# Kernel optimization log

Hardware: AMD Instinct MI355X
Metric: run time of the kernel (lower is better)

The kernel has to match this reference:

```python
import jax, jax.numpy as jnp
import numpy as np

B, C, W, H = 4, 256, 64, 64
D = C // 8  # reduced query/key channels


def setup_inputs() -> dict:
    key = jax.random.key(0)
    k1, k2, k3, k4, k5 = jax.random.split(key, 5)
    return {
        "x": jax.random.normal(k1, (B, C, W, H), dtype=jnp.float32),
        "q_weight": jax.random.normal(k2, (D, C), dtype=jnp.float32) * 0.05,
        "k_weight": jax.random.normal(k3, (D, C), dtype=jnp.float32) * 0.05,
        "v_weight": jax.random.normal(k4, (C, C), dtype=jnp.float32) * 0.05,
        "gamma": jax.random.normal(k5, (1,), dtype=jnp.float32),
    }


def reference(x, q_weight, k_weight, v_weight, gamma):
    b, c, w, h = x.shape
    n = w * h
    xf = x.reshape(b, c, n)                       # (B, C, N)
    # 1x1 convs == channel matmuls
    q = jnp.einsum('dc,bcn->bdn', q_weight, xf)   # (B, D, N)
    k = jnp.einsum('dc,bcn->bdn', k_weight, xf)   # (B, D, N)
    v = jnp.einsum('oc,bcn->bon', v_weight, xf)   # (B, C, N)
    # energy[b, i, j] = <q[:, i], k[:, j]>  (unscaled, single head)
    energy = jnp.einsum('bdi,bdj->bij', q, k)     # (B, N, N)
    attn = jax.nn.softmax(energy, axis=-1)        # softmax over keys j
    # out[b, c, i] = sum_j v[b, c, j] * attn[b, i, j]
    out = jnp.einsum('bcj,bij->bci', v, attn)     # (B, C, N)
    out = out.reshape(b, c, w, h)
    return gamma[0] * out + x
```

## Files before the change

kernel.cpp:

```cpp
#include <hip/hip_runtime.h>
#include <math.h>

#define Bb 4
#define Cc 256
#define Nn 4096
#define Dd 32
#define CH 128
#define XST 264

typedef __attribute__((ext_vector_type(8))) short bf16x8;
typedef __attribute__((ext_vector_type(4))) float f32x4;

__device__ __forceinline__ unsigned short f2bf(float x) {
    union { float f; unsigned u; } c; c.f = x;
    unsigned r = c.u + 0x7fffu + ((c.u >> 16) & 1u);
    return (unsigned short)(r >> 16);
}
__device__ __forceinline__ unsigned pk2(float a, float b) {
    return (unsigned)f2bf(a) | ((unsigned)f2bf(b) << 16);
}
__device__ __forceinline__ void load_lds16(const void* g, void* l) {
    __builtin_amdgcn_global_load_lds(
        (const __attribute__((address_space(1))) void*)g,
        (__attribute__((address_space(3))) void*)l, 16, 0, 0);
}
__device__ __forceinline__ float fexp2(float x) {
#if __has_builtin(__builtin_amdgcn_exp2f)
    return __builtin_amdgcn_exp2f(x);
#else
    return __exp2f(x);
#endif
}
template <int CTRL>
__device__ __forceinline__ float dppf(float v) {
    int iv = __builtin_bit_cast(int, v);
    return __builtin_bit_cast(float,
        __builtin_amdgcn_update_dpp(iv, iv, CTRL, 0xF, 0xF, false));
}
__device__ __forceinline__ float rowsum16(float v) {
    v += dppf<0xB1>(v);
    v += dppf<0x4E>(v);
    v += dppf<0x141>(v);
    v += dppf<0x140>(v);
    return v;
}

__global__ __launch_bounds__(256) void pack_w(
    const float* __restrict__ qw, const float* __restrict__ kw,
    const float* __restrict__ vw, short* __restrict__ wpk) {
    const int g = blockIdx.x * 256 + threadIdx.x;
    const int qd = g & 3, m = (g >> 2) & 15, kc = (g >> 6) & 7, ot = g >> 9;
    const int o = 16 * ot + m;
    const float* src;
    float scale = 1.0f;
    if (o < 32)      { src = qw + (size_t)o * Cc; scale = 1.44269504088896f; }
    else if (o < 64) { src = kw + (size_t)(o - 32) * Cc; }
    else             { src = vw + (size_t)(o - 64) * Cc; }
    const float* s8 = src + 32 * kc + 8 * qd;
    uint4 u;
    u.x = pk2(s8[0] * scale, s8[1] * scale);
    u.y = pk2(s8[2] * scale, s8[3] * scale);
    u.z = pk2(s8[4] * scale, s8[5] * scale);
    u.w = pk2(s8[6] * scale, s8[7] * scale);
    *(uint4*)(wpk + (size_t)g * 8) = u;
}

__global__ __launch_bounds__(256) void proj(
    const float* __restrict__ x, const short* __restrict__ wpk,
    short* __restrict__ q_t, short* __restrict__ k_t, short* __restrict__ v_b) {
    __shared__ alignas(16) short xs[32 * XST];
    const int b = blockIdx.z;
    const int n0 = blockIdx.x * 32;
    const int tid = threadIdx.x;
    const int w = tid >> 6;
    const int lane = tid & 63, qd = lane >> 4, m = lane & 15;

    {
        const int n = tid & 31, cg = tid >> 5;
        const float* xp = x + ((size_t)b * Cc + 32 * cg) * Nn + n0 + n;
        float xv[32];
#pragma unroll
        for (int i = 0; i < 32; ++i) xv[i] = xp[(size_t)i * Nn];
        short* row = xs + n * XST + 32 * cg;
#pragma unroll
        for (int u4 = 0; u4 < 4; ++u4)
            *(uint4*)(row + 8 * u4) = make_uint4(
                pk2(xv[8*u4+0], xv[8*u4+1]), pk2(xv[8*u4+2], xv[8*u4+3]),
                pk2(xv[8*u4+4], xv[8*u4+5]), pk2(xv[8*u4+6], xv[8*u4+7]));
    }
    __syncthreads();

    const int fslot = m * 4 + qd;
    f32x4 acc[5][2];
#pragma unroll
    for (int i = 0; i < 5; ++i)
#pragma unroll
        for (int nt = 0; nt < 2; ++nt) acc[i][nt] = (f32x4){0.f, 0.f, 0.f, 0.f};

    bf16x8 afc[5], afn[5];
#pragma unroll
    for (int i = 0; i < 5; ++i)
        afc[i] = *(const bf16x8*)(wpk + ((size_t)((4*i + w) * 8 + 0) * 64 + fslot) * 8);

    for (int kc = 0; kc < 8; ++kc) {
        if (kc < 7) {
#pragma unroll
            for (int i = 0; i < 5; ++i)
                afn[i] = *(const bf16x8*)(
                    wpk + ((size_t)((4*i + w) * 8 + kc + 1) * 64 + fslot) * 8);
        }
        const bf16x8 b0 = *(const bf16x8*)&xs[(     m) * XST + 32 * kc + 8 * qd];
        const bf16x8 b1 = *(const bf16x8*)&xs[(16 + m) * XST + 32 * kc + 8 * qd];
#pragma unroll
        for (int i = 0; i < 5; ++i)
            acc[i][0] = __builtin_amdgcn_mfma_f32_16x16x32_bf16(afc[i], b0, acc[i][0], 0, 0, 0);
#pragma unroll
        for (int i = 0; i < 5; ++i)
            acc[i][1] = __builtin_amdgcn_mfma_f32_16x16x32_bf16(afc[i], b1, acc[i][1], 0, 0, 0);
#pragma unroll
        for (int i = 0; i < 5; ++i) afc[i] = afn[i];
    }

#pragma unroll
    for (int i = 0; i < 5; ++i) {
        const int ot = 4 * i + w;
        if (ot < 4) {
            short* dst = (ot < 2 ? q_t : k_t) + (size_t)b * Nn * Dd;
            const int dbase = (ot & 1) * 16 + 4 * qd;
#pragma unroll
            for (int nt = 0; nt < 2; ++nt) {
                const f32x4 a = acc[i][nt];
                *(uint2*)(dst + (size_t)(n0 + 16 * nt + m) * Dd + dbase) =
                    make_uint2(pk2(a[0], a[1]), pk2(a[2], a[3]));
            }
        } else {
            const int cbase = (ot - 4) * 16 + 4 * qd;
            const int gbase = n0 & ~63;
            const int off2 = (n0 & 32) ? 2 : 0;
#pragma unroll
            for (int rr = 0; rr < 4; ++rr) {
                const unsigned pv = pk2(acc[i][0][rr], acc[i][1][rr]);
                *(unsigned*)(v_b + ((size_t)b * Cc + cbase + rr) * Nn +
                             gbase + 4 * m + off2) = pv;
            }
        }
    }
}

__global__ __launch_bounds__(256) void attn(
    const float* __restrict__ x, const short* __restrict__ q_t,
    const short* __restrict__ k_t, const short* __restrict__ v_b,
    const float* __restrict__ gamma, float* __restrict__ out) {
    __shared__ alignas(16) char pool[54528];
    short* q_s = (short*)(pool);
    char*  kv0 = pool + 4096;
    char*  kv1 = pool + 24576;
    short* p_s = (short*)(pool + 45056);
    float* l_s = (float*)(pool + 54272);
    float* o_t = (float*)(pool + 4096);

    const int b = blockIdx.z, cg = blockIdx.y;
    const int i0 = blockIdx.x * 64;
    const int tid = threadIdx.x;
    const int w = tid >> 6, lane = tid & 63;
    const int qd = lane >> 4, m = lane & 15;

    const short* ktb = k_t + (size_t)b * Nn * Dd;
    const short* vtb = v_b + ((size_t)(b * Cc) + cg * CH) * Nn;

    load_lds16(q_t + ((size_t)b * Nn + i0) * Dd + tid * 8, q_s + tid * 8);
    {
        load_lds16(ktb + tid * 8, kv0 + tid * 16);
        short* vls = (short*)(kv0 + 4096);
#pragma unroll
        for (int p = 0; p < 4; ++p) {
            const int cl = 32 * p + (tid >> 3);
            const int j8 = (tid & 7) ^ (cl & 7);
            load_lds16(vtb + (size_t)cl * Nn + j8 * 8, vls + 2048 * p + tid * 8);
        }
    }
    __syncthreads();

    const bf16x8 af = *(const bf16x8*)(q_s + (16 * w + m) * Dd + 8 * qd);

    f32x4 oacc[4][2];
#pragma unroll
    for (int mt = 0; mt < 4; ++mt)
#pragma unroll
        for (int nt = 0; nt < 2; ++nt) oacc[mt][nt] = (f32x4){0.f, 0.f, 0.f, 0.f};
    float l_i[4] = {0.f, 0.f, 0.f, 0.f};

    int cur = 0;
    for (int jt = 0; jt < Nn / 64; ++jt) {
        const char* kvc = cur ? kv1 : kv0;
        const short* k_s = (const short*)kvc;
        const short* v_s = (const short*)(kvc + 4096);

        if (jt) __syncthreads();

        f32x4 sf[4];
#pragma unroll
        for (int nt = 0; nt < 4; ++nt) {
            const bf16x8 bfr = *(const bf16x8*)(k_s + (16 * nt + m) * Dd + 8 * qd);
            sf[nt] = __builtin_amdgcn_mfma_f32_16x16x32_bf16(
                af, bfr, (f32x4){0.f, 0.f, 0.f, 0.f}, 0, 0, 0);
        }

#pragma unroll
        for (int rr = 0; rr < 4; ++rr) {
            float p0 = fexp2(sf[0][rr]);
            float p1 = fexp2(sf[1][rr]);
            float p2 = fexp2(sf[2][rr]);
            float p3 = fexp2(sf[3][rr]);
            l_i[rr] += (p0 + p1) + (p2 + p3);
            *(uint2*)&p_s[(16 * w + 4 * qd + rr) * 72 + 4 * m] =
                make_uint2(pk2(p0, p1), pk2(p2, p3));
        }
        __syncthreads();

        if (jt + 1 < Nn / 64) {
            char* kvn = cur ? kv0 : kv1;
            const int j0n = (jt + 1) * 64;
            load_lds16(ktb + (size_t)j0n * Dd + tid * 8, kvn + tid * 16);
            short* vls = (short*)(kvn + 4096);
#pragma unroll
            for (int p = 0; p < 4; ++p) {
                const int cl = 32 * p + (tid >> 3);
                const int j8 = (tid & 7) ^ (cl & 7);
                load_lds16(vtb + (size_t)cl * Nn + j0n + j8 * 8,
                           vls + 2048 * p + tid * 8);
            }
        }

#pragma unroll
        for (int kc = 0; kc < 2; ++kc) {
            bf16x8 pa[4];
#pragma unroll
            for (int mt = 0; mt < 4; ++mt)
                pa[mt] = *(const bf16x8*)&p_s[(16 * mt + m) * 72 + 32 * kc + 8 * qd];
#pragma unroll
            for (int nt = 0; nt < 2; ++nt) {
                const int cl = 32 * w + 16 * nt + m;
                const bf16x8 vb8 = *(const bf16x8*)(
                    v_s + cl * 64 + (((qd + 4 * kc) ^ (cl & 7)) * 8));
#pragma unroll
                for (int mt = 0; mt < 4; ++mt)
                    oacc[mt][nt] = __builtin_amdgcn_mfma_f32_16x16x32_bf16(
                        pa[mt], vb8, oacc[mt][nt], 0, 0, 0);
            }
        }
        cur ^= 1;
    }

#pragma unroll
    for (int rr = 0; rr < 4; ++rr) l_i[rr] = rowsum16(l_i[rr]);
    if (m == 0)
        *(f32x4*)&l_s[16 * w + 4 * qd] = (f32x4){l_i[0], l_i[1], l_i[2], l_i[3]};

    const float g = gamma[0];
#pragma unroll
    for (int ntp = 0; ntp < 2; ++ntp) {
        __syncthreads();
#pragma unroll
        for (int mt = 0; mt < 4; ++mt)
#pragma unroll
            for (int rr = 0; rr < 4; ++rr)
                o_t[(16 * mt + 4 * qd + rr) * 68 + 16 * w + m] = oacc[mt][ntp][rr];
        __syncthreads();
        const int i = lane;
        const float linv = 1.0f / l_s[i];
#pragma unroll
        for (int kk = 0; kk < 16; ++kk) {
            const int cp = w * 16 + kk;
            const int c = cg * CH + 32 * w + 16 * ntp + kk;
            const float val = o_t[i * 68 + cp] * linv;
            const size_t gidx = ((size_t)b * Cc + c) * Nn + i0 + i;
            out[gidx] = g * val + x[gidx];
        }
    }
}

extern "C" void kernel_launch(void* const* d_in, const int* in_sizes, int n_in,
                              void* d_out, int out_size, void* d_ws, size_t ws_size,
                              hipStream_t stream) {
    const float* x     = (const float*)d_in[0];
    const float* qw    = (const float*)d_in[1];
    const float* kw    = (const float*)d_in[2];
    const float* vw    = (const float*)d_in[3];
    const float* gamma = (const float*)d_in[4];
    float* out = (float*)d_out;

    short* q_t = (short*)d_ws;
    short* k_t = q_t + (size_t)Bb * Nn * Dd;
    short* v_b = k_t + (size_t)Bb * Nn * Dd;
    short* wpk = v_b + (size_t)Bb * Cc * Nn;

    pack_w<<<dim3(40), 256, 0, stream>>>(qw, kw, vw, wpk);
    proj<<<dim3(Nn / 32, 1, Bb), 256, 0, stream>>>(x, wpk, q_t, k_t, v_b);
    attn<<<dim3(Nn / 64, Cc / CH, Bb), 256, 0, stream>>>(x, q_t, k_t, v_b,
                                                         gamma, out);
}
```

Before: 153.5 us.

## Restructure pipeline: transpose x in prep, widen proj tiles, stream V via registers

Merges weight packing with a new x-to-bf16 transposed staging kernel, so proj reads a pre-transposed bf16 x_t and computes 64 columns per block instead of 32. The attention kernel now processes 128 keys per iteration. It keeps only K in LDS and loads V fragments straight from global memory into registers, double-buffered, which cuts LDS use so two blocks can fit per CU. It also uses a cheaper perm-based bf16 rounding and a flattened grid that groups the two channel halves of a batch next to each other. The costs are an extra full write and read of x_t, higher register pressure, and uncoalesced per-lane V loads.

```diff
diff --git a/kernel.cpp b/kernel.cpp
--- a/kernel.cpp
+++ b/kernel.cpp
@@ -6,18 +6,19 @@
 #define Nn 4096
 #define Dd 32
 #define CH 128
-#define XST 264
+#define NJ 32
+#define PST 136
+#define TPD 35
 
 typedef __attribute__((ext_vector_type(8))) short bf16x8;
 typedef __attribute__((ext_vector_type(4))) float f32x4;
 
-__device__ __forceinline__ unsigned short f2bf(float x) {
-    union { float f; unsigned u; } c; c.f = x;
-    unsigned r = c.u + 0x7fffu + ((c.u >> 16) & 1u);
-    return (unsigned short)(r >> 16);
-}
-__device__ __forceinline__ unsigned pk2(float a, float b) {
-    return (unsigned)f2bf(a) | ((unsigned)f2bf(b) << 16);
+union bfp { bf16x8 v; uint4 q; };
+
+__device__ __forceinline__ unsigned pk2r(float a, float b) {
+    unsigned au = __builtin_bit_cast(unsigned, a) + 0x8000u;
+    unsigned bu = __builtin_bit_cast(unsigned, b) + 0x8000u;
+    return __builtin_amdgcn_perm(bu, au, 0x07060302u);
 }
 __device__ __forceinline__ void load_lds16(const void* g, void* l) {
     __builtin_amdgcn_global_load_lds(
@@ -45,80 +46,90 @@
     return v;
 }
 
-__global__ __launch_bounds__(256) void pack_w(
-    const float* __restrict__ qw, const float* __restrict__ kw,
-    const float* __restrict__ vw, short* __restrict__ wpk) {
-    const int g = blockIdx.x * 256 + threadIdx.x;
-    const int qd = g & 3, m = (g >> 2) & 15, kc = (g >> 6) & 7, ot = g >> 9;
-    const int o = 16 * ot + m;
-    const float* src;
-    float scale = 1.0f;
-    if (o < 32)      { src = qw + (size_t)o * Cc; scale = 1.44269504088896f; }
-    else if (o < 64) { src = kw + (size_t)(o - 32) * Cc; }
-    else             { src = vw + (size_t)(o - 64) * Cc; }
-    const float* s8 = src + 32 * kc + 8 * qd;
-    uint4 u;
-    u.x = pk2(s8[0] * scale, s8[1] * scale);
-    u.y = pk2(s8[2] * scale, s8[3] * scale);
-    u.z = pk2(s8[4] * scale, s8[5] * scale);
-    u.w = pk2(s8[6] * scale, s8[7] * scale);
-    *(uint4*)(wpk + (size_t)g * 8) = u;
+__global__ __launch_bounds__(256) void prep(
+    const float* __restrict__ x, const float* __restrict__ qw,
+    const float* __restrict__ kw, const float* __restrict__ vw,
+    short* __restrict__ x_t, short* __restrict__ wpk) {
+    const int tid = threadIdx.x;
+    if (blockIdx.y == 4) {
+        if (blockIdx.z != 0 || blockIdx.x >= 40) return;
+        const int g = blockIdx.x * 256 + tid;
+        const int qd = g & 3, m = (g >> 2) & 15, kc = (g >> 6) & 7, ot = g >> 9;
+        const int o = 16 * ot + m;
+        const float* src; float sc = 1.0f;
+        if (o < 32)      { src = qw + (size_t)o * Cc; sc = 1.44269504088896f; }
+        else if (o < 64) { src = kw + (size_t)(o - 32) * Cc; }
+        else             { src = vw + (size_t)(o - 64) * Cc; }
+        const float* s8 = src + 32 * kc + 8 * qd;
+        uint4 u;
+        u.x = pk2r(s8[0] * sc, s8[1] * sc);
+        u.y = pk2r(s8[2] * sc, s8[3] * sc);
+        u.z = pk2r(s8[4] * sc, s8[5] * sc);
+        u.w = pk2r(s8[6] * sc, s8[7] * sc);
+        *(uint4*)(wpk + (size_t)g * 8) = u;
+        return;
+    }
+    __shared__ unsigned t_s[64 * TPD];
+    const int b = blockIdx.z;
+    const int n0 = blockIdx.x * 64, c0 = blockIdx.y * 64;
+    const int w = tid >> 6, lane = tid & 63;
+    {
+        const float* xb = x + ((size_t)b * Cc + c0) * Nn + n0 + lane;
+#pragma unroll
+        for (int i = 0; i < 8; ++i) {
+            const int cp = 8 * w + i;
+            const float v0 = xb[(size_t)(2 * cp) * Nn];
+            const float v1 = xb[(size_t)(2 * cp + 1) * Nn];
+            t_s[lane * TPD + cp] = pk2r(v0, v1);
+        }
+    }
+    __syncthreads();
+#pragma unroll
+    for (int r = 0; r < 4; ++r) {
+        const int idx = tid + 256 * r;
+        const int n = idx >> 4, u2 = idx & 15;
+        uint2 d;
+        d.x = t_s[n * TPD + 2 * u2];
+        d.y = t_s[n * TPD + 2 * u2 + 1];
+        *(uint2*)(x_t + ((size_t)b * Nn + n0 + n) * Cc + c0 + 4 * u2) = d;
+    }
 }
 
 __global__ __launch_bounds__(256) void proj(
-    const float* __restrict__ x, const short* __restrict__ wpk,
+    const short* __restrict__ x_t, const short* __restrict__ wpk,
     short* __restrict__ q_t, short* __restrict__ k_t, short* __restrict__ v_b) {
-    __shared__ alignas(16) short xs[32 * XST];
     const int b = blockIdx.z;
-    const int n0 = blockIdx.x * 32;
+    const int n0 = blockIdx.x * 64;
     const int tid = threadIdx.x;
-    const int w = tid >> 6;
-    const int lane = tid & 63, qd = lane >> 4, m = lane & 15;
-
-    {
-        const int n = tid & 31, cg = tid >> 5;
-        const float* xp = x + ((size_t)b * Cc + 32 * cg) * Nn + n0 + n;
-        float xv[32];
-#pragma unroll
-        for (int i = 0; i < 32; ++i) xv[i] = xp[(size_t)i * Nn];
-        short* row = xs + n * XST + 32 * cg;
-#pragma unroll
-        for (int u4 = 0; u4 < 4; ++u4)
-            *(uint4*)(row + 8 * u4) = make_uint4(
-                pk2(xv[8*u4+0], xv[8*u4+1]), pk2(xv[8*u4+2], xv[8*u4+3]),
-                pk2(xv[8*u4+4], xv[8*u4+5]), pk2(xv[8*u4+6], xv[8*u4+7]));
-    }
-    __syncthreads();
-
+    const int w = tid >> 6, lane = tid & 63;
+    const int qd = lane >> 4, m = lane & 15;
     const int fslot = m * 4 + qd;
-    f32x4 acc[5][2];
+
+    const short* xtb = x_t + ((size_t)b * Nn + n0) * Cc;
+
+    f32x4 acc[5][4];
 #pragma unroll
     for (int i = 0; i < 5; ++i)
 #pragma unroll
-        for (int nt = 0; nt < 2; ++nt) acc[i][nt] = (f32x4){0.f, 0.f, 0.f, 0.f};
-
-    bf16x8 afc[5], afn[5];
-#pragma unroll
-    for (int i = 0; i < 5; ++i)
-        afc[i] = *(const bf16x8*)(wpk + ((size_t)((4*i + w) * 8 + 0) * 64 + fslot) * 8);
-
+        for (int nt = 0; nt < 4; ++nt) acc[i][nt] = (f32x4){0.f, 0.f, 0.f, 0.f};
+
+#pragma unroll 2
     for (int kc = 0; kc < 8; ++kc) {
-        if (kc < 7) {
-#pragma unroll
-            for (int i = 0; i < 5; ++i)
-                afn[i] = *(const bf16x8*)(
-                    wpk + ((size_t)((4*i + w) * 8 + kc + 1) * 64 + fslot) * 8);
-        }
-        const bf16x8 b0 = *(const bf16x8*)&xs[(     m) * XST + 32 * kc + 8 * qd];
-        const bf16x8 b1 = *(const bf16x8*)&xs[(16 + m) * XST + 32 * kc + 8 * qd];
-#pragma unroll
-        for (int i = 0; i < 5; ++i)
-            acc[i][0] = __builtin_amdgcn_mfma_f32_16x16x32_bf16(afc[i], b0, acc[i][0], 0, 0, 0);
-#pragma unroll
-        for (int i = 0; i < 5; ++i)
-            acc[i][1] = __builtin_amdgcn_mfma_f32_16x16x32_bf16(afc[i], b1, acc[i][1], 0, 0, 0);
-#pragma unroll
-        for (int i = 0; i < 5; ++i) afc[i] = afn[i];
+        bfp bfr[4];
+#pragma unroll
+        for (int nt = 0; nt < 4; ++nt)
+            bfr[nt].q = *(const uint4*)(xtb + (size_t)(16 * nt + m) * Cc +
+                                        32 * kc + 8 * qd);
+#pragma unroll
+        for (int i = 0; i < 5; ++i) {
+            bfp af;
+            af.q = *(const uint4*)(wpk +
+                    ((size_t)((4 * i + w) * 8 + kc) * 64 + fslot) * 8);
+#pragma unroll
+            for (int nt = 0; nt < 4; ++nt)
+                acc[i][nt] = __builtin_amdgcn_mfma_f32_16x16x32_bf16(
+                    af.v, bfr[nt].v, acc[i][nt], 0, 0, 0);
+        }
     }
 
 #pragma unroll
@@ -128,128 +139,127 @@
             short* dst = (ot < 2 ? q_t : k_t) + (size_t)b * Nn * Dd;
             const int dbase = (ot & 1) * 16 + 4 * qd;
 #pragma unroll
-            for (int nt = 0; nt < 2; ++nt) {
+            for (int nt = 0; nt < 4; ++nt) {
                 const f32x4 a = acc[i][nt];
                 *(uint2*)(dst + (size_t)(n0 + 16 * nt + m) * Dd + dbase) =
-                    make_uint2(pk2(a[0], a[1]), pk2(a[2], a[3]));
+                    make_uint2(pk2r(a[0], a[1]), pk2r(a[2], a[3]));
             }
         } else {
-            const int cbase = (ot - 4) * 16 + 4 * qd;
-            const int gbase = n0 & ~63;
-            const int off2 = (n0 & 32) ? 2 : 0;
-#pragma unroll
-            for (int rr = 0; rr < 4; ++rr) {
-                const unsigned pv = pk2(acc[i][0][rr], acc[i][1][rr]);
-                *(unsigned*)(v_b + ((size_t)b * Cc + cbase + rr) * Nn +
-                             gbase + 4 * m + off2) = pv;
-            }
-        }
-    }
-}
-
-__global__ __launch_bounds__(256) void attn(
+            const int crow = (ot - 4) * 16 + 4 * qd;
+#pragma unroll
+            for (int rr = 0; rr < 4; ++rr)
+                *(uint2*)(v_b + ((size_t)b * Cc + crow + rr) * Nn + n0 + 4 * m) =
+                    make_uint2(pk2r(acc[i][0][rr], acc[i][1][rr]),
+                               pk2r(acc[i][2][rr], acc[i][3][rr]));
+        }
+    }
+}
+
+__global__ __launch_bounds__(256, 2) void attn(
     const float* __restrict__ x, const short* __restrict__ q_t,
     const short* __restrict__ k_t, const short* __restrict__ v_b,
     const float* __restrict__ gamma, float* __restrict__ out) {
-    __shared__ alignas(16) char pool[54528];
+    __shared__ alignas(16) char pool[38144];
     short* q_s = (short*)(pool);
-    char*  kv0 = pool + 4096;
-    char*  kv1 = pool + 24576;
-    short* p_s = (short*)(pool + 45056);
-    float* l_s = (float*)(pool + 54272);
-    float* o_t = (float*)(pool + 4096);
-
-    const int b = blockIdx.z, cg = blockIdx.y;
-    const int i0 = blockIdx.x * 64;
+    short* k0s = (short*)(pool + 4096);
+    short* k1s = (short*)(pool + 12288);
+    short* p_s = (short*)(pool + 20480);
+    float* l_s = (float*)(pool + 37888);
+    float* o_t = (float*)(pool + 20480);
+
+    const int bid = blockIdx.x;
+    const int b = (bid & 7) >> 1, cg = bid & 1;
+    const int i0 = (bid >> 3) * 64;
     const int tid = threadIdx.x;
     const int w = tid >> 6, lane = tid & 63;
     const int qd = lane >> 4, m = lane & 15;
 
     const short* ktb = k_t + (size_t)b * Nn * Dd;
     const short* vtb = v_b + ((size_t)(b * Cc) + cg * CH) * Nn;
+    const short* vr0 = vtb + (size_t)(32 * w + m) * Nn + 8 * qd;
+    const short* vr1 = vtb + (size_t)(32 * w + 16 + m) * Nn + 8 * qd;
 
     load_lds16(q_t + ((size_t)b * Nn + i0) * Dd + tid * 8, q_s + tid * 8);
-    {
-        load_lds16(ktb + tid * 8, kv0 + tid * 16);
-        short* vls = (short*)(kv0 + 4096);
-#pragma unroll
-        for (int p = 0; p < 4; ++p) {
-            const int cl = 32 * p + (tid >> 3);
-            const int j8 = (tid & 7) ^ (cl & 7);
-            load_lds16(vtb + (size_t)cl * Nn + j8 * 8, vls + 2048 * p + tid * 8);
-        }
+    load_lds16(ktb + tid * 8, k0s + tid * 8);
+    load_lds16(ktb + 2048 + tid * 8, k0s + 2048 + tid * 8);
+    uint4 va[8], vc[8];
+#pragma unroll
+    for (int kc = 0; kc < 4; ++kc) {
+        va[2 * kc]     = *(const uint4*)(vr0 + 32 * kc);
+        va[2 * kc + 1] = *(const uint4*)(vr1 + 32 * kc);
     }
     __syncthreads();
 
     const bf16x8 af = *(const bf16x8*)(q_s + (16 * w + m) * Dd + 8 * qd);
 
-    f32x4 oacc[4][2];
+    f32x4 acc[4][2];
 #pragma unroll
     for (int mt = 0; mt < 4; ++mt)
 #pragma unroll
-        for (int nt = 0; nt < 2; ++nt) oacc[mt][nt] = (f32x4){0.f, 0.f, 0.f, 0.f};
+        for (int nt = 0; nt < 2; ++nt) acc[mt][nt] = (f32x4){0.f, 0.f, 0.f, 0.f};
     float l_i[4] = {0.f, 0.f, 0.f, 0.f};
 
-    int cur = 0;
-    for (int jt = 0; jt < Nn / 64; ++jt) {
-        const char* kvc = cur ? kv1 : kv0;
-        const short* k_s = (const short*)kvc;
-        const short* v_s = (const short*)(kvc + 4096);
-
-        if (jt) __syncthreads();
-
-        f32x4 sf[4];
-#pragma unroll
-        for (int nt = 0; nt < 4; ++nt) {
-            const bf16x8 bfr = *(const bf16x8*)(k_s + (16 * nt + m) * Dd + 8 * qd);
+    auto body = [&](int jt, const short* kcur, short* knext,
+                    uint4* vcur, uint4* vnext) {
+        __syncthreads();
+
+        f32x4 sf[8];
+#pragma unroll
+        for (int nt = 0; nt < 8; ++nt) {
+            bfp kf;
+            kf.q = *(const uint4*)(kcur + (16 * nt + m) * Dd + 8 * qd);
             sf[nt] = __builtin_amdgcn_mfma_f32_16x16x32_bf16(
-                af, bfr, (f32x4){0.f, 0.f, 0.f, 0.f}, 0, 0, 0);
-        }
-
+                af, kf.v, (f32x4){0.f, 0.f, 0.f, 0.f}, 0, 0, 0);
+        }
 #pragma unroll
         for (int rr = 0; rr < 4; ++rr) {
-            float p0 = fexp2(sf[0][rr]);
-            float p1 = fexp2(sf[1][rr]);
-            float p2 = fexp2(sf[2][rr]);
-            float p3 = fexp2(sf[3][rr]);
-            l_i[rr] += (p0 + p1) + (p2 + p3);
-            *(uint2*)&p_s[(16 * w + 4 * qd + rr) * 72 + 4 * m] =
-                make_uint2(pk2(p0, p1), pk2(p2, p3));
+            float p[8];
+            float s = 0.f;
+#pragma unroll
+            for (int nt = 0; nt < 8; ++nt) { p[nt] = fexp2(sf[nt][rr]); s += p[nt]; }
+            l_i[rr] += s;
+            const int prow = (16 * w + 4 * qd + rr) * PST;
+            *(uint2*)&p_s[prow + 4 * m] =
+                make_uint2(pk2r(p[0], p[1]), pk2r(p[2], p[3]));
+            *(uint2*)&p_s[prow + 64 + 4 * m] =
+                make_uint2(pk2r(p[4], p[5]), pk2r(p[6], p[7]));
         }
         __syncthreads();
 
-        if (jt + 1 < Nn / 64) {
-            char* kvn = cur ? kv0 : kv1;
-            const int j0n = (jt + 1) * 64;
-            load_lds16(ktb + (size_t)j0n * Dd + tid * 8, kvn + tid * 16);
-            short* vls = (short*)(kvn + 4096);
-#pragma unroll
-            for (int p = 0; p < 4; ++p) {
-                const int cl = 32 * p + (tid >> 3);
-                const int j8 = (tid & 7) ^ (cl & 7);
-                load_lds16(vtb + (size_t)cl * Nn + j0n + j8 * 8,
-                           vls + 2048 * p + tid * 8);
+        if (jt + 1 < NJ) {
+            const size_t ko = (size_t)(jt + 1) * 4096;
+            load_lds16(ktb + ko + tid * 8, knext + tid * 8);
+            load_lds16(ktb + ko + 2048 + tid * 8, knext + 2048 + tid * 8);
+            const int joff = 128 * (jt + 1);
+#pragma unroll
+            for (int kc = 0; kc < 4; ++kc) {
+                vnext[2 * kc]     = *(const uint4*)(vr0 + joff + 32 * kc);
+                vnext[2 * kc + 1] = *(const uint4*)(vr1 + joff + 32 * kc);
             }
         }
-
-#pragma unroll
-        for (int kc = 0; kc < 2; ++kc) {
+#pragma unroll
+        for (int kc = 0; kc < 4; ++kc) {
             bf16x8 pa[4];
 #pragma unroll
-            for (int mt = 0; mt < 4; ++mt)
-                pa[mt] = *(const bf16x8*)&p_s[(16 * mt + m) * 72 + 32 * kc + 8 * qd];
+            for (int mt = 0; mt < 4; ++mt) {
+                bfp t;
+                t.q = *(const uint4*)&p_s[(16 * mt + m) * PST + 32 * kc + 8 * qd];
+                pa[mt] = t.v;
+            }
 #pragma unroll
             for (int nt = 0; nt < 2; ++nt) {
-                const int cl = 32 * w + 16 * nt + m;
-                const bf16x8 vb8 = *(const bf16x8*)(
-                    v_s + cl * 64 + (((qd + 4 * kc) ^ (cl & 7)) * 8));
+                bfp vv; vv.q = vcur[2 * kc + nt];
 #pragma unroll
                 for (int mt = 0; mt < 4; ++mt)
-                    oacc[mt][nt] = __builtin_amdgcn_mfma_f32_16x16x32_bf16(
-                        pa[mt], vb8, oacc[mt][nt], 0, 0, 0);
+                    acc[mt][nt] = __builtin_amdgcn_mfma_f32_16x16x32_bf16(
+                        pa[mt], vv.v, acc[mt][nt], 0, 0, 0);
             }
         }
-        cur ^= 1;
+    };
+
+    for (int jt = 0; jt < NJ; jt += 2) {
+        body(jt, k0s, k1s, va, vc);
+        body(jt + 1, k1s, k0s, vc, va);
     }
 
 #pragma unroll
@@ -265,7 +275,7 @@
         for (int mt = 0; mt < 4; ++mt)
 #pragma unroll
             for (int rr = 0; rr < 4; ++rr)
-                o_t[(16 * mt + 4 * qd + rr) * 68 + 16 * w + m] = oacc[mt][ntp][rr];
+                o_t[(16 * mt + 4 * qd + rr) * 68 + 16 * w + m] = acc[mt][ntp][rr];
         __syncthreads();
         const int i = lane;
         const float linv = 1.0f / l_s[i];
@@ -293,10 +303,10 @@
     short* q_t = (short*)d_ws;
     short* k_t = q_t + (size_t)Bb * Nn * Dd;
     short* v_b = k_t + (size_t)Bb * Nn * Dd;
-    short* wpk = v_b + (size_t)Bb * Cc * Nn;
-
-    pack_w<<<dim3(40), 256, 0, stream>>>(qw, kw, vw, wpk);
-    proj<<<dim3(Nn / 32, 1, Bb), 256, 0, stream>>>(x, wpk, q_t, k_t, v_b);
-    attn<<<dim3(Nn / 64, Cc / CH, Bb), 256, 0, stream>>>(x, q_t, k_t, v_b,
-                                                         gamma, out);
-}
+    short* x_t = v_b + (size_t)Bb * Cc * Nn;
+    short* wpk = x_t + (size_t)Bb * Nn * Cc;
+
+    prep<<<dim3(64, 5, Bb), 256, 0, stream>>>(x, qw, kw, vw, x_t, wpk);
+    proj<<<dim3(64, 1, Bb), 256, 0, stream>>>(x_t, wpk, q_t, k_t, v_b);
+    attn<<<dim3(512, 1, 1), 256, 0, stream>>>(x, q_t, k_t, v_b, gamma, out);
+}
```

New measurement: 164.8 us. 7.4% more time.
